# Optimization experiments

Measured on AMD Instinct MI355X. Metric: run time of the kernel, lower is better.

Reference implementation:

```python
import jax, jax.numpy as jnp
import numpy as np

N, K, H, E_IN = 4096, 48, 128, 384
SCALE = 30.0
EPS = 1e-5


def _gelu(x):
    return jax.nn.gelu(x, approximate=False)


def _ln(x, s, o):
    m = jnp.mean(x, axis=-1, keepdims=True)
    v = jnp.var(x, axis=-1, keepdims=True)
    return (x - m) * jax.lax.rsqrt(v + EPS) * s + o


def setup_inputs() -> dict:
    key = jax.random.key(0)
    ks = jax.random.split(key, 12)
    init = lambda k, shp: (jax.random.normal(k, shp, jnp.float32) * 0.02)
    return {
        "h_V": jax.random.normal(ks[0], (N, H), jnp.float32),
        "h_E": jax.random.normal(ks[1], (N, K, E_IN), jnp.float32),
        "mask_V": jnp.ones((N,), jnp.float32),
        "mask_attend": jnp.ones((N, K), jnp.float32),
        "W1_w": init(ks[2], (H + E_IN, H)), "W1_b": jnp.zeros((H,), jnp.float32),
        "W2_w": init(ks[3], (H, H)), "W2_b": jnp.zeros((H,), jnp.float32),
        "W3_w": init(ks[4], (H, H)), "W3_b": jnp.zeros((H,), jnp.float32),
        "Win_w": init(ks[5], (H, 4 * H)), "Win_b": jnp.zeros((4 * H,), jnp.float32),
        "Wout_w": init(ks[6], (4 * H, H)), "Wout_b": jnp.zeros((H,), jnp.float32),
        "norm1_s": jnp.ones((H,), jnp.float32), "norm1_o": jnp.zeros((H,), jnp.float32),
        "norm2_s": jnp.ones((H,), jnp.float32), "norm2_o": jnp.zeros((H,), jnp.float32),
    }


def reference(h_V, h_E, mask_V, mask_attend,
              W1_w, W1_b, W2_w, W2_b, W3_w, W3_b,
              Win_w, Win_b, Wout_w, Wout_b,
              norm1_s, norm1_o, norm2_s, norm2_o):
    # expand node features over K neighbors and concat with edge features: [N,K,H+E_IN]
    h_V_expand = jnp.broadcast_to(h_V[:, None, :], (h_V.shape[0], h_E.shape[1], h_V.shape[1]))
    h_EV = jnp.concatenate([h_V_expand, h_E], axis=-1)
    # 3-layer GELU MLP on each edge token
    h = _gelu(jnp.einsum('nke,eh->nkh', h_EV, W1_w) + W1_b)
    h = _gelu(jnp.einsum('nkh,hg->nkg', h, W2_w) + W2_b)
    h_message = jnp.einsum('nkg,gh->nkh', h, W3_w) + W3_b
    # masked sum-reduce over neighbors
    h_message = mask_attend[..., None] * h_message
    dh = jnp.sum(h_message, axis=-2) / SCALE
    h_Vn = _ln(h_V + dh, norm1_s, norm1_o)  # dropout rate = 0.0 -> identity
    # position-wise FFN
    dh = _gelu(h_Vn @ Win_w + Win_b) @ Wout_w + Wout_b
    h_Vn = _ln(h_Vn + dh, norm2_s, norm2_o)
    return mask_V[:, None] * h_Vn
```

## Files before the change

### kernel.cpp

```cpp
#include <hip/hip_runtime.h>
#include <hip/hip_bf16.h>
#include <math.h>

typedef __attribute__((ext_vector_type(8))) __bf16 bf16x8;
typedef __attribute__((ext_vector_type(4))) float f32x4;

#define OFF_W1P    0
#define OFF_W2P    65536
#define OFF_W3P    81920
#define OFF_WINP   98304
#define OFF_WOUTP  163840
#define NPACK      229376
#define OFF_DH_BYTES 458752

__device__ __forceinline__ float gelu_f(float x) {
  float t = 1.5957691216f * x * (1.0f + 0.044715f * x * x);
  return __fdividef(x, 1.0f + __expf(-t));
}

__device__ __forceinline__ bf16x8 cvt8(float4 u, float4 v) {
  bf16x8 r;
  r[0] = (__bf16)u.x; r[1] = (__bf16)u.y; r[2] = (__bf16)u.z; r[3] = (__bf16)u.w;
  r[4] = (__bf16)v.x; r[5] = (__bf16)v.y; r[6] = (__bf16)v.z; r[7] = (__bf16)v.w;
  return r;
}

#define MFMA __builtin_amdgcn_mfma_f32_16x16x32_bf16

__global__ __launch_bounds__(256) void prep_kernel(
    const float* __restrict__ W1, const float* __restrict__ W2,
    const float* __restrict__ W3, const float* __restrict__ Wi,
    const float* __restrict__ Wo, __bf16* __restrict__ wsb)
{
  int i = blockIdx.x * 256 + threadIdx.x;
  float v;
  if (i < 65536) {
    int j = i;
    int jj = j & 7, ln = (j >> 3) & 63, n = (j >> 9) & 7, ks = j >> 12;
    int k = ks * 32 + (ln >> 4) * 8 + jj, h = n * 16 + (ln & 15);
    v = W1[k * 128 + h];
  } else if (i < 81920) {
    int j = i - 65536;
    int jj = j & 7, ln = (j >> 3) & 63, n = (j >> 9) & 7, ks = j >> 12;
    int k = ks * 32 + (ln >> 4) * 8 + jj, g = n * 16 + (ln & 15);
    v = W2[k * 128 + g];
  } else if (i < 98304) {
    int j = i - 81920;
    int jj = j & 7, ln = (j >> 3) & 63, n = (j >> 9) & 7, ks = j >> 12;
    int k = ks * 32 + (ln >> 4) * 8 + jj, h = n * 16 + (ln & 15);
    v = W3[k * 128 + h];
  } else if (i < 163840) {
    int j = i - 98304;
    int jj = j & 7, ln = (j >> 3) & 63, n = (j >> 9) & 31, ks = j >> 14;
    int k = ks * 32 + (ln >> 4) * 8 + jj, o = n * 16 + (ln & 15);
    v = Wi[k * 512 + o];
  } else {
    int j = i - 163840;
    int jj = j & 7, ln = (j >> 3) & 63, n = (j >> 9) & 7, ks = j >> 12;
    int k = ks * 32 + (ln >> 4) * 8 + jj, h = n * 16 + (ln & 15);
    v = Wo[k * 128 + h];
  }
  wsb[i] = (__bf16)v;
}

__global__ __launch_bounds__(256, 4) void edge_mlp_kernel(
    const float* __restrict__ hE, const float* __restrict__ hV,
    const float* __restrict__ mask_att, const __bf16* __restrict__ wsb,
    const float* __restrict__ b1, const float* __restrict__ b2,
    const float* __restrict__ b3, float* __restrict__ dh)
{
  __shared__ char lds[24576];

  const int tid = threadIdx.x;
  const int w = tid >> 6, lane = tid & 63;
  const int lo = lane & 15, hi = lane >> 4;
  const int n0 = blockIdx.x * 2;

  const __bf16* W1p = wsb + OFF_W1P;

  f32x4 acc[2][3][2];
#pragma unroll
  for (int nl = 0; nl < 2; nl++)
#pragma unroll
    for (int m = 0; m < 3; m++)
#pragma unroll
      for (int nn = 0; nn < 2; nn++) {
        acc[nl][m][nn][0] = 0.f; acc[nl][m][nn][1] = 0.f;
        acc[nl][m][nn][2] = 0.f; acc[nl][m][nn][3] = 0.f;
      }

  const float* tsrc[3];
  int tdst[3];
#pragma unroll
  for (int p = 0; p < 3; p++) {
    int s = p * 256 + tid;
    int row = s >> 3, c8 = s & 7;
    int nl = (row >= 48) ? 1 : 0, kk = row - nl * 48;
    tsrc[p] = hE + ((size_t)((n0 + nl) * 48 + kk)) * 384 + c8 * 8;
    tdst[p] = row * 128 + ((c8 * 16) ^ ((row & 7) << 4));
  }

  float4 f1[3], f2[3];
#pragma unroll
  for (int p = 0; p < 3; p++) { f1[p] = *(const float4*)(tsrc[p]); f2[p] = *(const float4*)(tsrc[p] + 4); }

#pragma unroll 1
  for (int kc = 0; kc < 2; ++kc) {
#pragma unroll
    for (int ks32 = 0; ks32 < 2; ++ks32) {
      int ks = kc * 2 + ks32;
      const float* v0 = hV + (n0)     * 128 + ks * 32 + hi * 8;
      const float* v1 = hV + (n0 + 1) * 128 + ks * 32 + hi * 8;
      bf16x8 a0 = cvt8(*(const float4*)v0, *(const float4*)(v0 + 4));
      bf16x8 a1 = cvt8(*(const float4*)v1, *(const float4*)(v1 + 4));
#pragma unroll
      for (int nn = 0; nn < 2; nn++) {
        bf16x8 b = *(const bf16x8*)(W1p + ((ks * 8 + w * 2 + nn) << 9) + lane * 8);
#pragma unroll
        for (int m = 0; m < 3; m++) {
          acc[0][m][nn] = MFMA(a0, b, acc[0][m][nn], 0, 0, 0);
          acc[1][m][nn] = MFMA(a1, b, acc[1][m][nn], 0, 0, 0);
        }
      }
    }
#pragma unroll
    for (int p = 0; p < 3; p++)
      *(bf16x8*)(lds + kc * 12288 + tdst[p]) = cvt8(f1[p], f2[p]);
    if (kc == 0) {
#pragma unroll
      for (int p = 0; p < 3; p++) { f1[p] = *(const float4*)(tsrc[p] + 64); f2[p] = *(const float4*)(tsrc[p] + 68); }
    }
  }

#pragma unroll 1
  for (int kc = 2; kc < 8; ++kc) {
    if (kc < 6) {
      const int of = kc * 64;
#pragma unroll
      for (int p = 0; p < 3; p++) { f1[p] = *(const float4*)(tsrc[p] + of); f2[p] = *(const float4*)(tsrc[p] + of + 4); }
    }
    __syncthreads();
    {
      const char* Ab = lds + (kc & 1) * 12288;
#pragma unroll
      for (int ks32 = 0; ks32 < 2; ++ks32) {
        int ks = kc * 2 + ks32;
        bf16x8 bb[2];
#pragma unroll
        for (int nn = 0; nn < 2; nn++)
          bb[nn] = *(const bf16x8*)(W1p + ((ks * 8 + w * 2 + nn) << 9) + lane * 8);
        bf16x8 a[2][3];
#pragma unroll
        for (int nl = 0; nl < 2; nl++)
#pragma unroll
          for (int m = 0; m < 3; m++) {
            int row = nl * 48 + m * 16 + lo;
            a[nl][m] = *(const bf16x8*)(Ab + row * 128 + ((ks32 * 64 + hi * 16) ^ ((row & 7) << 4)));
          }
#pragma unroll
        for (int nn = 0; nn < 2; nn++)
#pragma unroll
          for (int nl = 0; nl < 2; nl++)
#pragma unroll
            for (int m = 0; m < 3; m++)
              acc[nl][m][nn] = MFMA(a[nl][m], bb[nn], acc[nl][m][nn], 0, 0, 0);
      }
    }
    __syncthreads();
    if (kc < 6) {
#pragma unroll
      for (int p = 0; p < 3; p++)
        *(bf16x8*)(lds + (kc & 1) * 12288 + tdst[p]) = cvt8(f1[p], f2[p]);
    }
  }

#pragma unroll 1
  for (int layer = 0; layer < 2; ++layer) {
    const float*  bv = layer ? b2 : b1;
    const __bf16* Wp = wsb + (layer ? OFF_W3P : OFF_W2P);
    __syncthreads();
#pragma unroll
    for (int nn = 0; nn < 2; nn++) {
      int col = (w * 2 + nn) * 16 + lo;
      float bc = bv[col];
#pragma unroll
      for (int nl = 0; nl < 2; nl++)
#pragma unroll
        for (int m = 0; m < 3; m++)
#pragma unroll
          for (int i = 0; i < 4; i++) {
            int row = nl * 48 + m * 16 + hi * 4 + i;
            float g = gelu_f(acc[nl][m][nn][i] + bc);
            *(__bf16*)(lds + row * 256 + ((col * 2) ^ ((row & 7) << 4))) = (__bf16)g;
            acc[nl][m][nn][i] = 0.f;
          }
    }
    __syncthreads();
#pragma unroll 1
    for (int kc2 = 0; kc2 < 2; ++kc2) {
#pragma unroll
      for (int ks32 = 0; ks32 < 2; ++ks32) {
        int ks = kc2 * 2 + ks32;
        bf16x8 bb[2];
#pragma unroll
        for (int nn = 0; nn < 2; nn++)
          bb[nn] = *(const bf16x8*)(Wp + ((ks * 8 + w * 2 + nn) << 9) + lane * 8);
        bf16x8 a[2][3];
#pragma unroll
        for (int nl = 0; nl < 2; nl++)
#pragma unroll
          for (int m = 0; m < 3; m++) {
            int row = nl * 48 + m * 16 + lo;
            a[nl][m] = *(const bf16x8*)(lds + row * 256 + ((kc2 * 128 + ks32 * 64 + hi * 16) ^ ((row & 7) << 4)));
          }
#pragma unroll
        for (int nn = 0; nn < 2; nn++)
#pragma unroll
          for (int nl = 0; nl < 2; nl++)
#pragma unroll
            for (int m = 0; m < 3; m++)
              acc[nl][m][nn] = MFMA(a[nl][m], bb[nn], acc[nl][m][nn], 0, 0, 0);
      }
    }
  }

#pragma unroll
  for (int nl = 0; nl < 2; nl++) {
    float msk[12];
#pragma unroll
    for (int m = 0; m < 3; m++)
#pragma unroll
      for (int i = 0; i < 4; i++)
        msk[m * 4 + i] = mask_att[(n0 + nl) * 48 + m * 16 + hi * 4 + i];
#pragma unroll
    for (int nn = 0; nn < 2; nn++) {
      int col = (w * 2 + nn) * 16 + lo;
      float bc = b3[col];
      float s = 0.f;
#pragma unroll
      for (int m = 0; m < 3; m++)
#pragma unroll
        for (int i = 0; i < 4; i++)
          s += (acc[nl][m][nn][i] + bc) * msk[m * 4 + i];
      s += __shfl_xor(s, 16);
      s += __shfl_xor(s, 32);
      if (hi == 0)
        dh[(n0 + nl) * 128 + col] = s * (1.0f / 30.0f);
    }
  }
}

__global__ __launch_bounds__(256, 2) void node_ffn_kernel(
    const float* __restrict__ hV, const float* __restrict__ maskV,
    const __bf16* __restrict__ wsb, const float* __restrict__ dh,
    const float* __restrict__ Winb, const float* __restrict__ Woutb,
    const float* __restrict__ ns1, const float* __restrict__ no1,
    const float* __restrict__ ns2, const float* __restrict__ no2,
    float* __restrict__ out)
{
  __shared__ char lds2[36864];
  char*  xA  = lds2;
  float* hvn = (float*)(lds2 + 4096);
  char*  A2  = lds2 + 12288;
  float* red = (float*)(lds2 + 28672);

  const __bf16* Winp  = wsb + OFF_WINP;
  const __bf16* Woutp = wsb + OFF_WOUTP;

  const int tid = threadIdx.x;
  const int w = tid >> 6, lane = tid & 63;
  const int lo = lane & 15, hi = lane >> 4;
  const int n0 = blockIdx.x * 16;

  const int row = tid >> 4;
  const int sg  = tid & 15;
  const int node = n0 + row;

  {
    const float* pv = hV + node * 128 + sg * 8;
    const float* pd = dh + node * 128 + sg * 8;
    float4 a0 = *(const float4*)pv;
    float4 a1 = *(const float4*)(pv + 4);
    float4 d0 = *(const float4*)pd;
    float4 d1 = *(const float4*)(pd + 4);
    float x[8] = { a0.x + d0.x, a0.y + d0.y, a0.z + d0.z, a0.w + d0.w,
                   a1.x + d1.x, a1.y + d1.y, a1.z + d1.z, a1.w + d1.w };
    float s = 0.f, sq = 0.f;
#pragma unroll
    for (int j = 0; j < 8; j++) { s += x[j]; sq += x[j] * x[j]; }
#pragma unroll
    for (int off = 8; off >= 1; off >>= 1) { s += __shfl_xor(s, off); sq += __shfl_xor(sq, off); }
    float mean = s * (1.f / 128.f);
    float var  = sq * (1.f / 128.f) - mean * mean;
    float rs = rsqrtf(var + 1e-5f);
    bf16x8 vb;
    float yv[8];
#pragma unroll
    for (int j = 0; j < 8; j++) {
      int col = sg * 8 + j;
      float y = (x[j] - mean) * rs * ns1[col] + no1[col];
      yv[j] = y; vb[j] = (__bf16)y;
    }
    *(float4*)(hvn + row * 128 + sg * 8)     = make_float4(yv[0], yv[1], yv[2], yv[3]);
    *(float4*)(hvn + row * 128 + sg * 8 + 4) = make_float4(yv[4], yv[5], yv[6], yv[7]);
    *(bf16x8*)(xA + row * 256 + ((sg * 16) ^ ((row & 7) << 4))) = vb;
  }
  __syncthreads();

  f32x4 acc[8];
#pragma unroll
  for (int n = 0; n < 8; n++) { acc[n][0] = 0.f; acc[n][1] = 0.f; acc[n][2] = 0.f; acc[n][3] = 0.f; }
#pragma unroll
  for (int ks = 0; ks < 4; ks++) {
    const int kb = (ks * 32 + hi * 8) * 2;
    bf16x8 a = *(const bf16x8*)(xA + lo * 256 + (kb ^ ((lo & 7) << 4)));
#pragma unroll
    for (int n = 0; n < 8; n++) {
      int ng = w * 8 + n;
      bf16x8 b = *(const bf16x8*)(Winp + ((ks * 32 + ng) << 9) + lane * 8);
      acc[n] = MFMA(a, b, acc[n], 0, 0, 0);
    }
  }
#pragma unroll
  for (int n = 0; n < 8; n++) {
    int col = w * 128 + n * 16 + lo;
    float bc = Winb[col];
#pragma unroll
    for (int i = 0; i < 4; i++) {
      int r2 = hi * 4 + i;
      float g = gelu_f(acc[n][i] + bc);
      *(__bf16*)(A2 + r2 * 1024 + ((col * 2) ^ ((r2 & 7) << 4))) = (__bf16)g;
    }
  }
  __syncthreads();

  f32x4 acc2[2];
  acc2[0][0] = 0.f; acc2[0][1] = 0.f; acc2[0][2] = 0.f; acc2[0][3] = 0.f;
  acc2[1][0] = 0.f; acc2[1][1] = 0.f; acc2[1][2] = 0.f; acc2[1][3] = 0.f;
#pragma unroll
  for (int ks = 0; ks < 16; ks++) {
    const int kb = (ks * 32 + hi * 8) * 2;
    bf16x8 a = *(const bf16x8*)(A2 + lo * 1024 + (kb ^ ((lo & 7) << 4)));
#pragma unroll
    for (int n = 0; n < 2; n++) {
      int ng = w * 2 + n;
      bf16x8 b = *(const bf16x8*)(Woutp + ((ks * 8 + ng) << 9) + lane * 8);
      acc2[n] = MFMA(a, b, acc2[n], 0, 0, 0);
    }
  }
#pragma unroll
  for (int n = 0; n < 2; n++) {
    int col = w * 32 + n * 16 + lo;
    float bc = Woutb[col];
#pragma unroll
    for (int i = 0; i < 4; i++) {
      int r2 = hi * 4 + i;
      red[r2 * 128 + col] = acc2[n][i] + bc;
    }
  }
  __syncthreads();

  {
    const float* ph = hvn + row * 128 + sg * 8;
    const float* pr = red + row * 128 + sg * 8;
    float4 h0 = *(const float4*)ph;
    float4 h1 = *(const float4*)(ph + 4);
    float4 r0 = *(const float4*)pr;
    float4 r1 = *(const float4*)(pr + 4);
    float x[8] = { h0.x + r0.x, h0.y + r0.y, h0.z + r0.z, h0.w + r0.w,
                   h1.x + r1.x, h1.y + r1.y, h1.z + r1.z, h1.w + r1.w };
    float s = 0.f, sq = 0.f;
#pragma unroll
    for (int j = 0; j < 8; j++) { s += x[j]; sq += x[j] * x[j]; }
#pragma unroll
    for (int off = 8; off >= 1; off >>= 1) { s += __shfl_xor(s, off); sq += __shfl_xor(sq, off); }
    float mean = s * (1.f / 128.f);
    float var  = sq * (1.f / 128.f) - mean * mean;
    float rs = rsqrtf(var + 1e-5f);
    float mv = maskV[node];
    float o[8];
#pragma unroll
    for (int j = 0; j < 8; j++) {
      int col = sg * 8 + j;
      o[j] = mv * ((x[j] - mean) * rs * ns2[col] + no2[col]);
    }
    *(float4*)(out + node * 128 + sg * 8)     = make_float4(o[0], o[1], o[2], o[3]);
    *(float4*)(out + node * 128 + sg * 8 + 4) = make_float4(o[4], o[5], o[6], o[7]);
  }
}

extern "C" void kernel_launch(void* const* d_in, const int* in_sizes, int n_in,
                              void* d_out, int out_size, void* d_ws, size_t ws_size,
                              hipStream_t stream)
{
  (void)in_sizes; (void)n_in; (void)out_size; (void)ws_size;
  const float* hV   = (const float*)d_in[0];
  const float* hE   = (const float*)d_in[1];
  const float* mV   = (const float*)d_in[2];
  const float* mAtt = (const float*)d_in[3];
  const float* W1   = (const float*)d_in[4];
  const float* b1   = (const float*)d_in[5];
  const float* W2   = (const float*)d_in[6];
  const float* b2   = (const float*)d_in[7];
  const float* W3   = (const float*)d_in[8];
  const float* b3   = (const float*)d_in[9];
  const float* Win  = (const float*)d_in[10];
  const float* binb = (const float*)d_in[11];
  const float* Wout = (const float*)d_in[12];
  const float* bout = (const float*)d_in[13];
  const float* ns1  = (const float*)d_in[14];
  const float* no1  = (const float*)d_in[15];
  const float* ns2  = (const float*)d_in[16];
  const float* no2  = (const float*)d_in[17];

  __bf16* wsb = (__bf16*)d_ws;
  float* dh   = (float*)((char*)d_ws + OFF_DH_BYTES);
  float* out  = (float*)d_out;

  prep_kernel<<<NPACK / 256, 256, 0, stream>>>(W1, W2, W3, Win, Wout, wsb);
  edge_mlp_kernel<<<2048, 256, 0, stream>>>(hE, hV, mAtt, wsb, b1, b2, b3, dh);
  node_ffn_kernel<<<256, 256, 0, stream>>>(hV, mV, wsb, dh, binb, bout,
                                           ns1, no1, ns2, no2, out);
}
```

Before: 110.6 us.

## Fuse node FFN into edge MLP kernel and restructure hE prefetch pipeline

```diff
diff --git a/kernel.cpp b/kernel.cpp
--- a/kernel.cpp
+++ b/kernel.cpp
@@ -11,7 +11,6 @@
 #define OFF_WINP   98304
 #define OFF_WOUTP  163840
 #define NPACK      229376
-#define OFF_DH_BYTES 458752
 
 __device__ __forceinline__ float gelu_f(float x) {
   float t = 1.5957691216f * x * (1.0f + 0.044715f * x * x);
@@ -23,6 +22,10 @@
   r[0] = (__bf16)u.x; r[1] = (__bf16)u.y; r[2] = (__bf16)u.z; r[3] = (__bf16)u.w;
   r[4] = (__bf16)v.x; r[5] = (__bf16)v.y; r[6] = (__bf16)v.z; r[7] = (__bf16)v.w;
   return r;
+}
+
+__device__ __forceinline__ void bar_lgkm() {
+  asm volatile("s_waitcnt lgkmcnt(0)\n\ts_barrier" ::: "memory");
 }
 
 #define MFMA __builtin_amdgcn_mfma_f32_16x16x32_bf16
@@ -63,11 +66,15 @@
   wsb[i] = (__bf16)v;
 }
 
-__global__ __launch_bounds__(256, 4) void edge_mlp_kernel(
+__global__ __launch_bounds__(256, 3) void edge_mlp_kernel(
     const float* __restrict__ hE, const float* __restrict__ hV,
     const float* __restrict__ mask_att, const __bf16* __restrict__ wsb,
     const float* __restrict__ b1, const float* __restrict__ b2,
-    const float* __restrict__ b3, float* __restrict__ dh)
+    const float* __restrict__ b3,
+    const float* __restrict__ Winb, const float* __restrict__ Woutb,
+    const float* __restrict__ ns1, const float* __restrict__ no1,
+    const float* __restrict__ ns2, const float* __restrict__ no2,
+    const float* __restrict__ maskV, float* __restrict__ out)
 {
   __shared__ char lds[24576];
 
@@ -100,51 +107,61 @@
     tdst[p] = row * 128 + ((c8 * 16) ^ ((row & 7) << 4));
   }
 
-  float4 f1[3], f2[3];
-#pragma unroll
-  for (int p = 0; p < 3; p++) { f1[p] = *(const float4*)(tsrc[p]); f2[p] = *(const float4*)(tsrc[p] + 4); }
+  float4 f1[3], f2[3], g1[3], g2[3];
+#pragma unroll
+  for (int p = 0; p < 3; p++) { f1[p] = *(const float4*)(tsrc[p]);      f2[p] = *(const float4*)(tsrc[p] + 4); }
+#pragma unroll
+  for (int p = 0; p < 3; p++) { g1[p] = *(const float4*)(tsrc[p] + 64); g2[p] = *(const float4*)(tsrc[p] + 68); }
 
 #pragma unroll 1
-  for (int kc = 0; kc < 2; ++kc) {
-#pragma unroll
-    for (int ks32 = 0; ks32 < 2; ++ks32) {
-      int ks = kc * 2 + ks32;
-      const float* v0 = hV + (n0)     * 128 + ks * 32 + hi * 8;
-      const float* v1 = hV + (n0 + 1) * 128 + ks * 32 + hi * 8;
-      bf16x8 a0 = cvt8(*(const float4*)v0, *(const float4*)(v0 + 4));
-      bf16x8 a1 = cvt8(*(const float4*)v1, *(const float4*)(v1 + 4));
-#pragma unroll
-      for (int nn = 0; nn < 2; nn++) {
-        bf16x8 b = *(const bf16x8*)(W1p + ((ks * 8 + w * 2 + nn) << 9) + lane * 8);
-#pragma unroll
-        for (int m = 0; m < 3; m++) {
-          acc[0][m][nn] = MFMA(a0, b, acc[0][m][nn], 0, 0, 0);
-          acc[1][m][nn] = MFMA(a1, b, acc[1][m][nn], 0, 0, 0);
-        }
-      }
-    }
-#pragma unroll
-    for (int p = 0; p < 3; p++)
-      *(bf16x8*)(lds + kc * 12288 + tdst[p]) = cvt8(f1[p], f2[p]);
-    if (kc == 0) {
-#pragma unroll
-      for (int p = 0; p < 3; p++) { f1[p] = *(const float4*)(tsrc[p] + 64); f2[p] = *(const float4*)(tsrc[p] + 68); }
-    }
-  }
+  for (int ks = 0; ks < 4; ++ks) {
+    const float* v0 = hV + (n0)     * 128 + ks * 32 + hi * 8;
+    const float* v1 = hV + (n0 + 1) * 128 + ks * 32 + hi * 8;
+    bf16x8 a0 = cvt8(*(const float4*)v0, *(const float4*)(v0 + 4));
+    bf16x8 a1 = cvt8(*(const float4*)v1, *(const float4*)(v1 + 4));
+#pragma unroll
+    for (int nn = 0; nn < 2; nn++) {
+      bf16x8 b = *(const bf16x8*)(W1p + ((ks * 8 + w * 2 + nn) << 9) + lane * 8);
+#pragma unroll
+      for (int m = 0; m < 3; m++) {
+        acc[0][m][nn] = MFMA(a0, b, acc[0][m][nn], 0, 0, 0);
+        acc[1][m][nn] = MFMA(a1, b, acc[1][m][nn], 0, 0, 0);
+      }
+    }
+  }
+#pragma unroll
+  for (int p = 0; p < 3; p++)
+    *(bf16x8*)(lds + tdst[p]) = cvt8(f1[p], f2[p]);
+#pragma unroll
+  for (int p = 0; p < 3; p++) { f1[p] = *(const float4*)(tsrc[p] + 128); f2[p] = *(const float4*)(tsrc[p] + 132); }
+  bar_lgkm();
 
 #pragma unroll 1
-  for (int kc = 2; kc < 8; ++kc) {
-    if (kc < 6) {
-      const int of = kc * 64;
-#pragma unroll
-      for (int p = 0; p < 3; p++) { f1[p] = *(const float4*)(tsrc[p] + of); f2[p] = *(const float4*)(tsrc[p] + of + 4); }
-    }
-    __syncthreads();
+  for (int i = 0; i < 6; ++i) {
+    if (i < 5) {
+      if ((i & 1) == 0) {
+#pragma unroll
+        for (int p = 0; p < 3; p++) *(bf16x8*)(lds + 12288 - (i & 1) * 12288 + tdst[p]) = cvt8(g1[p], g2[p]);
+      } else {
+#pragma unroll
+        for (int p = 0; p < 3; p++) *(bf16x8*)(lds + 12288 - (i & 1) * 12288 + tdst[p]) = cvt8(f1[p], f2[p]);
+      }
+    }
+    if (i <= 2) {
+      const int of = (i + 3) * 64;
+      if ((i & 1) == 0) {
+#pragma unroll
+        for (int p = 0; p < 3; p++) { g1[p] = *(const float4*)(tsrc[p] + of); g2[p] = *(const float4*)(tsrc[p] + of + 4); }
+      } else {
+#pragma unroll
+        for (int p = 0; p < 3; p++) { f1[p] = *(const float4*)(tsrc[p] + of); f2[p] = *(const float4*)(tsrc[p] + of + 4); }
+      }
+    }
     {
-      const char* Ab = lds + (kc & 1) * 12288;
+      const char* Ab = lds + (i & 1) * 12288;
 #pragma unroll
       for (int ks32 = 0; ks32 < 2; ++ks32) {
-        int ks = kc * 2 + ks32;
+        int ks = 4 + i * 2 + ks32;
         bf16x8 bb[2];
 #pragma unroll
         for (int nn = 0; nn < 2; nn++)
@@ -166,12 +183,7 @@
               acc[nl][m][nn] = MFMA(a[nl][m], bb[nn], acc[nl][m][nn], 0, 0, 0);
       }
     }
-    __syncthreads();
-    if (kc < 6) {
-#pragma unroll
-      for (int p = 0; p < 3; p++)
-        *(bf16x8*)(lds + (kc & 1) * 12288 + tdst[p]) = cvt8(f1[p], f2[p]);
-    }
+    if (i < 5) bar_lgkm();
   }
 
 #pragma unroll 1
@@ -224,6 +236,15 @@
     }
   }
 
+  char*  xA    = lds;
+  float* hvnl  = (float*)(lds + 4096);
+  float* dhl   = (float*)(lds + 5120);
+  float* part  = (float*)(lds + 6144);
+  float* redl  = (float*)(lds + 6400);
+  char*  A2    = lds + 8192;
+
+  __syncthreads();
+
 #pragma unroll
   for (int nl = 0; nl < 2; nl++) {
     float msk[12];
@@ -245,147 +266,103 @@
       s += __shfl_xor(s, 16);
       s += __shfl_xor(s, 32);
       if (hi == 0)
-        dh[(n0 + nl) * 128 + col] = s * (1.0f / 30.0f);
-    }
-  }
-}
-
-__global__ __launch_bounds__(256, 2) void node_ffn_kernel(
-    const float* __restrict__ hV, const float* __restrict__ maskV,
-    const __bf16* __restrict__ wsb, const float* __restrict__ dh,
-    const float* __restrict__ Winb, const float* __restrict__ Woutb,
-    const float* __restrict__ ns1, const float* __restrict__ no1,
-    const float* __restrict__ ns2, const float* __restrict__ no2,
-    float* __restrict__ out)
-{
-  __shared__ char lds2[36864];
-  char*  xA  = lds2;
-  float* hvn = (float*)(lds2 + 4096);
-  char*  A2  = lds2 + 12288;
-  float* red = (float*)(lds2 + 28672);
-
-  const __bf16* Winp  = wsb + OFF_WINP;
-  const __bf16* Woutp = wsb + OFF_WOUTP;
-
-  const int tid = threadIdx.x;
-  const int w = tid >> 6, lane = tid & 63;
-  const int lo = lane & 15, hi = lane >> 4;
-  const int n0 = blockIdx.x * 16;
-
-  const int row = tid >> 4;
-  const int sg  = tid & 15;
-  const int node = n0 + row;
+        dhl[nl * 128 + col] = s * (1.0f / 30.0f);
+    }
+  }
+  if (tid < 224) { bf16x8 z = {}; *(bf16x8*)(xA + 512 + tid * 16) = z; }
+  __syncthreads();
 
   {
-    const float* pv = hV + node * 128 + sg * 8;
-    const float* pd = dh + node * 128 + sg * 8;
-    float4 a0 = *(const float4*)pv;
-    float4 a1 = *(const float4*)(pv + 4);
-    float4 d0 = *(const float4*)pd;
-    float4 d1 = *(const float4*)(pd + 4);
-    float x[8] = { a0.x + d0.x, a0.y + d0.y, a0.z + d0.z, a0.w + d0.w,
-                   a1.x + d1.x, a1.y + d1.y, a1.z + d1.z, a1.w + d1.w };
-    float s = 0.f, sq = 0.f;
-#pragma unroll
-    for (int j = 0; j < 8; j++) { s += x[j]; sq += x[j] * x[j]; }
-#pragma unroll
-    for (int off = 8; off >= 1; off >>= 1) { s += __shfl_xor(s, off); sq += __shfl_xor(sq, off); }
-    float mean = s * (1.f / 128.f);
-    float var  = sq * (1.f / 128.f) - mean * mean;
+    const int r = tid >> 7, c = tid & 127;
+    float x = hV[(n0 + r) * 128 + c] + dhl[r * 128 + c];
+    float s = x, sq = x * x;
+#pragma unroll
+    for (int off = 32; off >= 1; off >>= 1) { s += __shfl_xor(s, off); sq += __shfl_xor(sq, off); }
+    if (lane == 0) { part[w * 2] = s; part[w * 2 + 1] = sq; }
+    __syncthreads();
+    float st = part[4 * r] + part[4 * r + 2];
+    float sqt = part[4 * r + 1] + part[4 * r + 3];
+    float mean = st * (1.f / 128.f);
+    float var  = sqt * (1.f / 128.f) - mean * mean;
     float rs = rsqrtf(var + 1e-5f);
-    bf16x8 vb;
-    float yv[8];
-#pragma unroll
-    for (int j = 0; j < 8; j++) {
-      int col = sg * 8 + j;
-      float y = (x[j] - mean) * rs * ns1[col] + no1[col];
-      yv[j] = y; vb[j] = (__bf16)y;
-    }
-    *(float4*)(hvn + row * 128 + sg * 8)     = make_float4(yv[0], yv[1], yv[2], yv[3]);
-    *(float4*)(hvn + row * 128 + sg * 8 + 4) = make_float4(yv[4], yv[5], yv[6], yv[7]);
-    *(bf16x8*)(xA + row * 256 + ((sg * 16) ^ ((row & 7) << 4))) = vb;
+    float y = (x - mean) * rs * ns1[c] + no1[c];
+    hvnl[r * 128 + c] = y;
+    *(__bf16*)(xA + r * 256 + (((c >> 3) * 16) ^ (r << 4)) + (c & 7) * 2) = (__bf16)y;
   }
   __syncthreads();
 
-  f32x4 acc[8];
-#pragma unroll
-  for (int n = 0; n < 8; n++) { acc[n][0] = 0.f; acc[n][1] = 0.f; acc[n][2] = 0.f; acc[n][3] = 0.f; }
-#pragma unroll
-  for (int ks = 0; ks < 4; ks++) {
-    const int kb = (ks * 32 + hi * 8) * 2;
-    bf16x8 a = *(const bf16x8*)(xA + lo * 256 + (kb ^ ((lo & 7) << 4)));
+  {
+    const __bf16* Winp = wsb + OFF_WINP;
+    f32x4 acc1[8];
+#pragma unroll
+    for (int n = 0; n < 8; n++) { acc1[n][0] = 0.f; acc1[n][1] = 0.f; acc1[n][2] = 0.f; acc1[n][3] = 0.f; }
+#pragma unroll
+    for (int ks = 0; ks < 4; ks++) {
+      const int kb = (ks * 32 + hi * 8) * 2;
+      bf16x8 a = *(const bf16x8*)(xA + lo * 256 + (kb ^ ((lo & 7) << 4)));
+#pragma unroll
+      for (int n = 0; n < 8; n++) {
+        int ng = w * 8 + n;
+        bf16x8 b = *(const bf16x8*)(Winp + ((ks * 32 + ng) << 9) + lane * 8);
+        acc1[n] = MFMA(a, b, acc1[n], 0, 0, 0);
+      }
+    }
 #pragma unroll
     for (int n = 0; n < 8; n++) {
-      int ng = w * 8 + n;
-      bf16x8 b = *(const bf16x8*)(Winp + ((ks * 32 + ng) << 9) + lane * 8);
-      acc[n] = MFMA(a, b, acc[n], 0, 0, 0);
-    }
-  }
-#pragma unroll
-  for (int n = 0; n < 8; n++) {
-    int col = w * 128 + n * 16 + lo;
-    float bc = Winb[col];
-#pragma unroll
-    for (int i = 0; i < 4; i++) {
-      int r2 = hi * 4 + i;
-      float g = gelu_f(acc[n][i] + bc);
-      *(__bf16*)(A2 + r2 * 1024 + ((col * 2) ^ ((r2 & 7) << 4))) = (__bf16)g;
+      int col = w * 128 + n * 16 + lo;
+      float bc = Winb[col];
+#pragma unroll
+      for (int i = 0; i < 4; i++) {
+        int r2 = hi * 4 + i;
+        float g = gelu_f(acc1[n][i] + bc);
+        *(__bf16*)(A2 + r2 * 1024 + ((col * 2) ^ ((r2 & 7) << 4))) = (__bf16)g;
+      }
     }
   }
   __syncthreads();
 
-  f32x4 acc2[2];
-  acc2[0][0] = 0.f; acc2[0][1] = 0.f; acc2[0][2] = 0.f; acc2[0][3] = 0.f;
-  acc2[1][0] = 0.f; acc2[1][1] = 0.f; acc2[1][2] = 0.f; acc2[1][3] = 0.f;
-#pragma unroll
-  for (int ks = 0; ks < 16; ks++) {
-    const int kb = (ks * 32 + hi * 8) * 2;
-    bf16x8 a = *(const bf16x8*)(A2 + lo * 1024 + (kb ^ ((lo & 7) << 4)));
+  {
+    const __bf16* Woutp = wsb + OFF_WOUTP;
+    f32x4 acc2[2];
+    acc2[0][0] = 0.f; acc2[0][1] = 0.f; acc2[0][2] = 0.f; acc2[0][3] = 0.f;
+    acc2[1][0] = 0.f; acc2[1][1] = 0.f; acc2[1][2] = 0.f; acc2[1][3] = 0.f;
+#pragma unroll
+    for (int ks = 0; ks < 16; ks++) {
+      const int kb = (ks * 32 + hi * 8) * 2;
+      bf16x8 a = *(const bf16x8*)(A2 + lo * 1024 + (kb ^ ((lo & 7) << 4)));
+#pragma unroll
+      for (int n = 0; n < 2; n++) {
+        int ng = w * 2 + n;
+        bf16x8 b = *(const bf16x8*)(Woutp + ((ks * 8 + ng) << 9) + lane * 8);
+        acc2[n] = MFMA(a, b, acc2[n], 0, 0, 0);
+      }
+    }
 #pragma unroll
     for (int n = 0; n < 2; n++) {
-      int ng = w * 2 + n;
-      bf16x8 b = *(const bf16x8*)(Woutp + ((ks * 8 + ng) << 9) + lane * 8);
-      acc2[n] = MFMA(a, b, acc2[n], 0, 0, 0);
-    }
-  }
-#pragma unroll
-  for (int n = 0; n < 2; n++) {
-    int col = w * 32 + n * 16 + lo;
-    float bc = Woutb[col];
-#pragma unroll
-    for (int i = 0; i < 4; i++) {
-      int r2 = hi * 4 + i;
-      red[r2 * 128 + col] = acc2[n][i] + bc;
+      int col = w * 32 + n * 16 + lo;
+      float bc = Woutb[col];
+#pragma unroll
+      for (int i = 0; i < 2; i++)
+        if (hi == 0)
+          redl[i * 128 + col] = acc2[n][i] + bc;
     }
   }
   __syncthreads();
 
   {
-    const float* ph = hvn + row * 128 + sg * 8;
-    const float* pr = red + row * 128 + sg * 8;
-    float4 h0 = *(const float4*)ph;
-    float4 h1 = *(const float4*)(ph + 4);
-    float4 r0 = *(const float4*)pr;
-    float4 r1 = *(const float4*)(pr + 4);
-    float x[8] = { h0.x + r0.x, h0.y + r0.y, h0.z + r0.z, h0.w + r0.w,
-                   h1.x + r1.x, h1.y + r1.y, h1.z + r1.z, h1.w + r1.w };
-    float s = 0.f, sq = 0.f;
-#pragma unroll
-    for (int j = 0; j < 8; j++) { s += x[j]; sq += x[j] * x[j]; }
-#pragma unroll
-    for (int off = 8; off >= 1; off >>= 1) { s += __shfl_xor(s, off); sq += __shfl_xor(sq, off); }
-    float mean = s * (1.f / 128.f);
-    float var  = sq * (1.f / 128.f) - mean * mean;
+    const int r = tid >> 7, c = tid & 127;
+    float x = hvnl[r * 128 + c] + redl[r * 128 + c];
+    float s = x, sq = x * x;
+#pragma unroll
+    for (int off = 32; off >= 1; off >>= 1) { s += __shfl_xor(s, off); sq += __shfl_xor(sq, off); }
+    if (lane == 0) { part[w * 2] = s; part[w * 2 + 1] = sq; }
+    __syncthreads();
+    float st = part[4 * r] + part[4 * r + 2];
+    float sqt = part[4 * r + 1] + part[4 * r + 3];
+    float mean = st * (1.f / 128.f);
+    float var  = sqt * (1.f / 128.f) - mean * mean;
     float rs = rsqrtf(var + 1e-5f);
-    float mv = maskV[node];
-    float o[8];
-#pragma unroll
-    for (int j = 0; j < 8; j++) {
-      int col = sg * 8 + j;
-      o[j] = mv * ((x[j] - mean) * rs * ns2[col] + no2[col]);
-    }
-    *(float4*)(out + node * 128 + sg * 8)     = make_float4(o[0], o[1], o[2], o[3]);
-    *(float4*)(out + node * 128 + sg * 8 + 4) = make_float4(o[4], o[5], o[6], o[7]);
+    out[(n0 + r) * 128 + c] = maskV[n0 + r] * ((x - mean) * rs * ns2[c] + no2[c]);
   }
 }
 
@@ -414,11 +391,10 @@
   const float* no2  = (const float*)d_in[17];
 
   __bf16* wsb = (__bf16*)d_ws;
-  float* dh   = (float*)((char*)d_ws + OFF_DH_BYTES);
   float* out  = (float*)d_out;
 
   prep_kernel<<<NPACK / 256, 256, 0, stream>>>(W1, W2, W3, Win, Wout, wsb);
-  edge_mlp_kernel<<<2048, 256, 0, stream>>>(hE, hV, mAtt, wsb, b1, b2, b3, dh);
-  node_ffn_kernel<<<256, 256, 0, stream>>>(hV, mV, wsb, dh, binb, bout,
-                                           ns1, no1, ns2, no2, out);
-}
+  edge_mlp_kernel<<<2048, 256, 0, stream>>>(hE, hV, mAtt, wsb, b1, b2, b3,
+                                            binb, bout, ns1, no1, ns2, no2,
+                                            mV, out);
+}
```

Result: slower. 123.1 us (+11.3%).

## Deepen h_E prefetch to two stages with single barrier per chunk

Applied to the files above, without the earlier changes.

```diff
diff --git a/kernel.cpp b/kernel.cpp
--- a/kernel.cpp
+++ b/kernel.cpp
@@ -23,6 +23,10 @@
   r[0] = (__bf16)u.x; r[1] = (__bf16)u.y; r[2] = (__bf16)u.z; r[3] = (__bf16)u.w;
   r[4] = (__bf16)v.x; r[5] = (__bf16)v.y; r[6] = (__bf16)v.z; r[7] = (__bf16)v.w;
   return r;
+}
+
+__device__ __forceinline__ void bar_lgkm() {
+  asm volatile("s_waitcnt lgkmcnt(0)\n\ts_barrier" ::: "memory");
 }
 
 #define MFMA __builtin_amdgcn_mfma_f32_16x16x32_bf16
@@ -63,7 +67,7 @@
   wsb[i] = (__bf16)v;
 }
 
-__global__ __launch_bounds__(256, 4) void edge_mlp_kernel(
+__global__ __launch_bounds__(256, 3) void edge_mlp_kernel(
     const float* __restrict__ hE, const float* __restrict__ hV,
     const float* __restrict__ mask_att, const __bf16* __restrict__ wsb,
     const float* __restrict__ b1, const float* __restrict__ b2,
@@ -100,55 +104,67 @@
     tdst[p] = row * 128 + ((c8 * 16) ^ ((row & 7) << 4));
   }
 
-  float4 f1[3], f2[3];
-#pragma unroll
-  for (int p = 0; p < 3; p++) { f1[p] = *(const float4*)(tsrc[p]); f2[p] = *(const float4*)(tsrc[p] + 4); }
+  float4 pA1[3], pA2[3], pB1[3], pB2[3];
+#pragma unroll
+  for (int p = 0; p < 3; p++) { pA1[p] = *(const float4*)(tsrc[p]);      pA2[p] = *(const float4*)(tsrc[p] + 4); }
+#pragma unroll
+  for (int p = 0; p < 3; p++) { pB1[p] = *(const float4*)(tsrc[p] + 64); pB2[p] = *(const float4*)(tsrc[p] + 68); }
 
 #pragma unroll 1
-  for (int kc = 0; kc < 2; ++kc) {
-#pragma unroll
-    for (int ks32 = 0; ks32 < 2; ++ks32) {
-      int ks = kc * 2 + ks32;
-      const float* v0 = hV + (n0)     * 128 + ks * 32 + hi * 8;
-      const float* v1 = hV + (n0 + 1) * 128 + ks * 32 + hi * 8;
-      bf16x8 a0 = cvt8(*(const float4*)v0, *(const float4*)(v0 + 4));
-      bf16x8 a1 = cvt8(*(const float4*)v1, *(const float4*)(v1 + 4));
-#pragma unroll
-      for (int nn = 0; nn < 2; nn++) {
-        bf16x8 b = *(const bf16x8*)(W1p + ((ks * 8 + w * 2 + nn) << 9) + lane * 8);
-#pragma unroll
-        for (int m = 0; m < 3; m++) {
-          acc[0][m][nn] = MFMA(a0, b, acc[0][m][nn], 0, 0, 0);
-          acc[1][m][nn] = MFMA(a1, b, acc[1][m][nn], 0, 0, 0);
-        }
-      }
-    }
-#pragma unroll
-    for (int p = 0; p < 3; p++)
-      *(bf16x8*)(lds + kc * 12288 + tdst[p]) = cvt8(f1[p], f2[p]);
-    if (kc == 0) {
-#pragma unroll
-      for (int p = 0; p < 3; p++) { f1[p] = *(const float4*)(tsrc[p] + 64); f2[p] = *(const float4*)(tsrc[p] + 68); }
-    }
-  }
+  for (int ks = 0; ks < 4; ++ks) {
+    const float* v0 = hV + (n0)     * 128 + ks * 32 + hi * 8;
+    const float* v1 = hV + (n0 + 1) * 128 + ks * 32 + hi * 8;
+    bf16x8 a0 = cvt8(*(const float4*)v0, *(const float4*)(v0 + 4));
+    bf16x8 a1 = cvt8(*(const float4*)v1, *(const float4*)(v1 + 4));
+#pragma unroll
+    for (int nn = 0; nn < 2; nn++) {
+      bf16x8 b = *(const bf16x8*)(W1p + ((ks * 8 + w * 2 + nn) << 9) + lane * 8);
+#pragma unroll
+      for (int m = 0; m < 3; m++) {
+        acc[0][m][nn] = MFMA(a0, b, acc[0][m][nn], 0, 0, 0);
+        acc[1][m][nn] = MFMA(a1, b, acc[1][m][nn], 0, 0, 0);
+      }
+    }
+  }
+#pragma unroll
+  for (int p = 0; p < 3; p++)
+    *(bf16x8*)(lds + tdst[p]) = cvt8(pA1[p], pA2[p]);
+#pragma unroll
+  for (int p = 0; p < 3; p++) { pA1[p] = *(const float4*)(tsrc[p] + 128); pA2[p] = *(const float4*)(tsrc[p] + 132); }
+  bar_lgkm();
 
 #pragma unroll 1
-  for (int kc = 2; kc < 8; ++kc) {
-    if (kc < 6) {
-      const int of = kc * 64;
-#pragma unroll
-      for (int p = 0; p < 3; p++) { f1[p] = *(const float4*)(tsrc[p] + of); f2[p] = *(const float4*)(tsrc[p] + of + 4); }
-    }
-    __syncthreads();
+  for (int i = 0; i < 6; ++i) {
+    char* wbuf = lds + ((i + 1) & 1) * 12288;
+    if (i < 5) {
+      if (i & 1) {
+#pragma unroll
+        for (int p = 0; p < 3; p++) *(bf16x8*)(wbuf + tdst[p]) = cvt8(pA1[p], pA2[p]);
+      } else {
+#pragma unroll
+        for (int p = 0; p < 3; p++) *(bf16x8*)(wbuf + tdst[p]) = cvt8(pB1[p], pB2[p]);
+      }
+    }
+    bf16x8 bb[2][2];
+#pragma unroll
+    for (int ks32 = 0; ks32 < 2; ++ks32)
+#pragma unroll
+      for (int nn = 0; nn < 2; nn++)
+        bb[ks32][nn] = *(const bf16x8*)(W1p + (((4 + i * 2 + ks32) * 8 + w * 2 + nn) << 9) + lane * 8);
+    if (i <= 2) {
+      const int of = (i + 3) * 64;
+      if (i & 1) {
+#pragma unroll
+        for (int p = 0; p < 3; p++) { pA1[p] = *(const float4*)(tsrc[p] + of); pA2[p] = *(const float4*)(tsrc[p] + of + 4); }
+      } else {
+#pragma unroll
+        for (int p = 0; p < 3; p++) { pB1[p] = *(const float4*)(tsrc[p] + of); pB2[p] = *(const float4*)(tsrc[p] + of + 4); }
+      }
+    }
     {
-      const char* Ab = lds + (kc & 1) * 12288;
+      const char* Ab = lds + (i & 1) * 12288;
 #pragma unroll
       for (int ks32 = 0; ks32 < 2; ++ks32) {
-        int ks = kc * 2 + ks32;
-        bf16x8 bb[2];
-#pragma unroll
-        for (int nn = 0; nn < 2; nn++)
-          bb[nn] = *(const bf16x8*)(W1p + ((ks * 8 + w * 2 + nn) << 9) + lane * 8);
         bf16x8 a[2][3];
 #pragma unroll
         for (int nl = 0; nl < 2; nl++)
@@ -163,15 +179,10 @@
           for (int nl = 0; nl < 2; nl++)
 #pragma unroll
             for (int m = 0; m < 3; m++)
-              acc[nl][m][nn] = MFMA(a[nl][m], bb[nn], acc[nl][m][nn], 0, 0, 0);
-      }
-    }
-    __syncthreads();
-    if (kc < 6) {
-#pragma unroll
-      for (int p = 0; p < 3; p++)
-        *(bf16x8*)(lds + (kc & 1) * 12288 + tdst[p]) = cvt8(f1[p], f2[p]);
-    }
+              acc[nl][m][nn] = MFMA(a[nl][m], bb[ks32][nn], acc[nl][m][nn], 0, 0, 0);
+      }
+    }
+    if (i < 5) bar_lgkm();
   }
 
 #pragma unroll 1
```

After: 110.7 us. About the same (+0.0%).

## Stream h_E fp32 tiles directly into LDS via global_load_lds double buffering

Applied to the files above, without the earlier changes.

```diff
diff --git a/kernel.cpp b/kernel.cpp
--- a/kernel.cpp
+++ b/kernel.cpp
@@ -23,6 +23,12 @@
   r[0] = (__bf16)u.x; r[1] = (__bf16)u.y; r[2] = (__bf16)u.z; r[3] = (__bf16)u.w;
   r[4] = (__bf16)v.x; r[5] = (__bf16)v.y; r[6] = (__bf16)v.z; r[7] = (__bf16)v.w;
   return r;
+}
+
+__device__ __forceinline__ void gload_lds16(const void* g, void* l) {
+  __builtin_amdgcn_global_load_lds(
+      (const __attribute__((address_space(1))) void*)g,
+      (__attribute__((address_space(3))) void*)l, 16, 0, 0);
 }
 
 #define MFMA __builtin_amdgcn_mfma_f32_16x16x32_bf16
@@ -89,89 +95,88 @@
         acc[nl][m][nn][2] = 0.f; acc[nl][m][nn][3] = 0.f;
       }
 
-  const float* tsrc[3];
-  int tdst[3];
-#pragma unroll
-  for (int p = 0; p < 3; p++) {
-    int s = p * 256 + tid;
-    int row = s >> 3, c8 = s & 7;
-    int nl = (row >= 48) ? 1 : 0, kk = row - nl * 48;
-    tsrc[p] = hE + ((size_t)((n0 + nl) * 48 + kk)) * 384 + c8 * 8;
-    tdst[p] = row * 128 + ((c8 * 16) ^ ((row & 7) << 4));
-  }
-
-  float4 f1[3], f2[3];
-#pragma unroll
-  for (int p = 0; p < 3; p++) { f1[p] = *(const float4*)(tsrc[p]); f2[p] = *(const float4*)(tsrc[p] + 4); }
+  const char* gsrc[3];
+  int ldst[3];
+#pragma unroll
+  for (int j = 0; j < 3; j++) {
+    int o = w * 3072 + j * 1024 + lane * 16;
+    int r = o >> 7;
+    int p = (o >> 4) & 7;
+    int lcol = p ^ (r & 7);
+    int nl = (r >= 48) ? 1 : 0, kk = r - nl * 48;
+    gsrc[j] = (const char*)(hE + (size_t)((n0 + nl) * 48 + kk) * 384 + lcol * 4);
+    ldst[j] = w * 3072 + j * 1024;
+  }
+
+#pragma unroll
+  for (int j = 0; j < 3; j++) gload_lds16(gsrc[j],       &lds[ldst[j]]);
+#pragma unroll
+  for (int j = 0; j < 3; j++) gload_lds16(gsrc[j] + 128, &lds[12288 + ldst[j]]);
 
 #pragma unroll 1
-  for (int kc = 0; kc < 2; ++kc) {
-#pragma unroll
-    for (int ks32 = 0; ks32 < 2; ++ks32) {
-      int ks = kc * 2 + ks32;
-      const float* v0 = hV + (n0)     * 128 + ks * 32 + hi * 8;
-      const float* v1 = hV + (n0 + 1) * 128 + ks * 32 + hi * 8;
-      bf16x8 a0 = cvt8(*(const float4*)v0, *(const float4*)(v0 + 4));
-      bf16x8 a1 = cvt8(*(const float4*)v1, *(const float4*)(v1 + 4));
-#pragma unroll
-      for (int nn = 0; nn < 2; nn++) {
-        bf16x8 b = *(const bf16x8*)(W1p + ((ks * 8 + w * 2 + nn) << 9) + lane * 8);
-#pragma unroll
-        for (int m = 0; m < 3; m++) {
-          acc[0][m][nn] = MFMA(a0, b, acc[0][m][nn], 0, 0, 0);
-          acc[1][m][nn] = MFMA(a1, b, acc[1][m][nn], 0, 0, 0);
-        }
+  for (int ks = 0; ks < 4; ++ks) {
+    const float* v0 = hV + (n0)     * 128 + ks * 32 + hi * 8;
+    const float* v1 = hV + (n0 + 1) * 128 + ks * 32 + hi * 8;
+    bf16x8 a0 = cvt8(*(const float4*)v0, *(const float4*)(v0 + 4));
+    bf16x8 a1 = cvt8(*(const float4*)v1, *(const float4*)(v1 + 4));
+#pragma unroll
+    for (int nn = 0; nn < 2; nn++) {
+      bf16x8 b = *(const bf16x8*)(W1p + ((ks * 8 + w * 2 + nn) << 9) + lane * 8);
+#pragma unroll
+      for (int m = 0; m < 3; m++) {
+        acc[0][m][nn] = MFMA(a0, b, acc[0][m][nn], 0, 0, 0);
+        acc[1][m][nn] = MFMA(a1, b, acc[1][m][nn], 0, 0, 0);
       }
     }
-#pragma unroll
-    for (int p = 0; p < 3; p++)
-      *(bf16x8*)(lds + kc * 12288 + tdst[p]) = cvt8(f1[p], f2[p]);
-    if (kc == 0) {
-#pragma unroll
-      for (int p = 0; p < 3; p++) { f1[p] = *(const float4*)(tsrc[p] + 64); f2[p] = *(const float4*)(tsrc[p] + 68); }
-    }
-  }
+  }
+
+  bf16x8 bbc[2], bbn[2];
+#pragma unroll
+  for (int nn = 0; nn < 2; nn++)
+    bbc[nn] = *(const bf16x8*)(W1p + ((4 * 8 + w * 2 + nn) << 9) + lane * 8);
+
+  const int swz0 = (2 * hi) ^ (lo & 7);
+  const int swz1 = (2 * hi + 1) ^ (lo & 7);
 
 #pragma unroll 1
-  for (int kc = 2; kc < 8; ++kc) {
-    if (kc < 6) {
-      const int of = kc * 64;
-#pragma unroll
-      for (int p = 0; p < 3; p++) { f1[p] = *(const float4*)(tsrc[p] + of); f2[p] = *(const float4*)(tsrc[p] + of + 4); }
-    }
-    __syncthreads();
-    {
-      const char* Ab = lds + (kc & 1) * 12288;
-#pragma unroll
-      for (int ks32 = 0; ks32 < 2; ++ks32) {
-        int ks = kc * 2 + ks32;
-        bf16x8 bb[2];
-#pragma unroll
-        for (int nn = 0; nn < 2; nn++)
-          bb[nn] = *(const bf16x8*)(W1p + ((ks * 8 + w * 2 + nn) << 9) + lane * 8);
-        bf16x8 a[2][3];
-#pragma unroll
-        for (int nl = 0; nl < 2; nl++)
-#pragma unroll
-          for (int m = 0; m < 3; m++) {
-            int row = nl * 48 + m * 16 + lo;
-            a[nl][m] = *(const bf16x8*)(Ab + row * 128 + ((ks32 * 64 + hi * 16) ^ ((row & 7) << 4)));
-          }
-#pragma unroll
-        for (int nn = 0; nn < 2; nn++)
-#pragma unroll
-          for (int nl = 0; nl < 2; nl++)
-#pragma unroll
-            for (int m = 0; m < 3; m++)
-              acc[nl][m][nn] = MFMA(a[nl][m], bb[nn], acc[nl][m][nn], 0, 0, 0);
+  for (int i = 0; i < 12; ++i) {
+    if (i < 11) asm volatile("s_waitcnt vmcnt(3)\n\ts_barrier" ::: "memory");
+    else        asm volatile("s_waitcnt vmcnt(0)\n\ts_barrier" ::: "memory");
+
+    if (i < 11) {
+#pragma unroll
+      for (int nn = 0; nn < 2; nn++)
+        bbn[nn] = *(const bf16x8*)(W1p + (((5 + i) * 8 + w * 2 + nn) << 9) + lane * 8);
+    }
+
+    const char* Ab = lds + (i & 1) * 12288;
+    bf16x8 a[2][3];
+#pragma unroll
+    for (int nl = 0; nl < 2; nl++)
+#pragma unroll
+      for (int m = 0; m < 3; m++) {
+        int r = nl * 48 + m * 16 + lo;
+        const char* rb = Ab + r * 128;
+        float4 u = *(const float4*)(rb + swz0 * 16);
+        float4 v = *(const float4*)(rb + swz1 * 16);
+        a[nl][m] = cvt8(u, v);
       }
-    }
-    __syncthreads();
-    if (kc < 6) {
-#pragma unroll
-      for (int p = 0; p < 3; p++)
-        *(bf16x8*)(lds + (kc & 1) * 12288 + tdst[p]) = cvt8(f1[p], f2[p]);
-    }
+#pragma unroll
+    for (int nn = 0; nn < 2; nn++)
+#pragma unroll
+      for (int nl = 0; nl < 2; nl++)
+#pragma unroll
+        for (int m = 0; m < 3; m++)
+          acc[nl][m][nn] = MFMA(a[nl][m], bbc[nn], acc[nl][m][nn], 0, 0, 0);
+
+    asm volatile("s_waitcnt lgkmcnt(0)\n\ts_barrier" ::: "memory");
+    if (i < 10) {
+      const int of = (i + 2) * 128;
+#pragma unroll
+      for (int j = 0; j < 3; j++)
+        gload_lds16(gsrc[j] + of, &lds[(i & 1) * 12288 + ldst[j]]);
+    }
+    if (i < 11) { bbc[0] = bbn[0]; bbc[1] = bbn[1]; }
   }
 
 #pragma unroll 1
```

After: 111.8 us. Within noise of the previous version (+1.1%).
